# Kernel optimization log

Hardware: AMD Instinct MI355X
Metric: run time of the kernel (lower is better)

Reference implementation:

```python
import jax, jax.numpy as jnp
import numpy as np
import math

D_MODEL = 256
N_HEADS = 8
NUM_NODES = 20
KSIZE = 3
EPS = 1e-5


def _ln(x, g, b):
    m = jnp.mean(x, axis=-1, keepdims=True)
    v = jnp.mean(jnp.square(x - m), axis=-1, keepdims=True)
    return (x - m) * jax.lax.rsqrt(v + EPS) * g + b


def _conv1d(x_bdn, w_oik):
    # x: [B, D, N], w: [O, I, K], SAME padding, no bias
    return jax.lax.conv_general_dilated(
        x_bdn, w_oik, window_strides=(1,), padding='SAME',
        dimension_numbers=('NCH', 'OIH', 'NCH'))


def setup_inputs() -> dict:
    key = jax.random.key(0)
    ks = jax.random.split(key, 12)
    B, N, D, H, K = 8192, NUM_NODES, D_MODEL, N_HEADS, KSIZE
    s = 1.0 / math.sqrt(D * K)
    inp = {
        'x': jax.random.normal(ks[0], (B, N, D), jnp.float32),
        'wq': jax.random.normal(ks[1], (D, D, K), jnp.float32) * s,
        'wk': jax.random.normal(ks[2], (D, D, K), jnp.float32) * s,
        'wv': jax.random.normal(ks[3], (D, D, K), jnp.float32) * s,
        'gq': jnp.ones((D,), jnp.float32), 'bq': jnp.zeros((D,), jnp.float32),
        'gk': jnp.ones((D,), jnp.float32), 'bk': jnp.zeros((D,), jnp.float32),
        'gv': jnp.ones((D,), jnp.float32), 'bv': jnp.zeros((D,), jnp.float32),
        'rel_table': jax.random.normal(ks[4], (2 * N - 1, H), jnp.float32) * 0.02,
        'gbias': jax.random.normal(ks[5], (H, N, N), jnp.float32) * 0.02,
        'alpha': jnp.float32(1.0),
        'wo': jax.random.normal(ks[6], (D, D), jnp.float32) * (1.0 / math.sqrt(D)),
        'bo': jnp.zeros((D,), jnp.float32),
    }
    return inp


def reference(x, wq, wk, wv, gq, bq, gk, bk, gv, bv, rel_table, gbias, alpha, wo, bo):
    B, N, D = x.shape
    H = N_HEADS
    dk = D // H
    xp = jnp.transpose(x, (0, 2, 1))  # [B, D, N]
    q = x + _ln(jnp.transpose(_conv1d(xp, wq), (0, 2, 1)), gq, bq)
    k = x + _ln(jnp.transpose(_conv1d(xp, wk), (0, 2, 1)), gk, bk)
    v = x + _ln(jnp.transpose(_conv1d(xp, wv), (0, 2, 1)), gv, bv)
    q = q.reshape(B, N, H, dk).transpose(0, 2, 1, 3)  # [B, H, N, dk]
    k = k.reshape(B, N, H, dk).transpose(0, 2, 1, 3)
    v = v.reshape(B, N, H, dk).transpose(0, 2, 1, 3)
    scores = jnp.einsum('bhnd,bhmd->bhnm', q, k) / math.sqrt(dk)
    # relative position bias: index table [2N-1, H] -> [1, H, N, N]
    coords = jnp.arange(N)
    rel_idx = coords[:, None] - coords[None, :] + N - 1  # [N, N]
    rel_bias = rel_table[rel_idx]  # [N, N, H]
    scores = scores + jnp.transpose(rel_bias, (2, 0, 1))[None]
    scores = scores + gbias[None] * alpha
    attn = jax.nn.softmax(scores, axis=-1)
    out = jnp.einsum('bhnm,bhmd->bhnd', attn, v)  # dropout p=0
    out = out.transpose(0, 2, 1, 3).reshape(B, N, D)
    return out @ wo.T + bo
```

## Files before the change

kernel.cpp:

```cpp
#include <hip/hip_runtime.h>
#include <hip/hip_bf16.h>
#include <stdint.h>

#define BATCH 8192
#define NNODE 20
#define MROWS 163840
#define KCONV 768
#define NCONV 768
#define QSCALE 0.17677669529663687f

typedef __bf16 bf16x8 __attribute__((ext_vector_type(8)));
typedef float f32x4 __attribute__((ext_vector_type(4)));
typedef unsigned short u16x8 __attribute__((ext_vector_type(8)));

#define GLOBAL_AS __attribute__((address_space(1)))
#define LDS_AS __attribute__((address_space(3)))

__device__ __forceinline__ void load_lds16(const void* g, void* l) {
  __builtin_amdgcn_global_load_lds((const GLOBAL_AS uint32_t*)g,
                                   (LDS_AS uint32_t*)l, 16, 0, 0);
}

__device__ __forceinline__ float bf2f(unsigned short u) {
  union { unsigned int i; float f; } x;
  x.i = ((unsigned int)u) << 16;
  return x.f;
}

__global__ void prep_kernel(const float* __restrict__ x,
                            const float* __restrict__ wq,
                            const float* __restrict__ wk,
                            const float* __restrict__ wv,
                            const float* __restrict__ wo,
                            __hip_bfloat16* __restrict__ xb,
                            __hip_bfloat16* __restrict__ WcT,
                            __hip_bfloat16* __restrict__ wob,
                            int* __restrict__ zrow) {
  const int stride = gridDim.x * blockDim.x;
  const int gid = blockIdx.x * blockDim.x + threadIdx.x;

  if (gid < 128) zrow[gid] = 0;

  const int n8 = (MROWS * 256) / 8;
  for (int i8 = gid; i8 < n8; i8 += stride) {
    const float4* xp = ((const float4*)x) + (size_t)i8 * 2;
    float4 a = xp[0];
    float4 b = xp[1];
    __align__(16) __hip_bfloat16 h[8];
    h[0] = __float2bfloat16(a.x); h[1] = __float2bfloat16(a.y);
    h[2] = __float2bfloat16(a.z); h[3] = __float2bfloat16(a.w);
    h[4] = __float2bfloat16(b.x); h[5] = __float2bfloat16(b.y);
    h[6] = __float2bfloat16(b.z); h[7] = __float2bfloat16(b.w);
    ((int4*)xb)[i8] = *(const int4*)h;
  }

  for (int idx = gid; idx < NCONV * KCONV; idx += stride) {
    int n = idx / KCONV;
    int j = idx - n * KCONV;
    int c = n >> 8, o = n & 255;
    int t = j >> 8, i = j & 255;
    const float* w = (c == 0) ? wq : (c == 1) ? wk : wv;
    WcT[idx] = __float2bfloat16(w[(o * 256 + i) * 3 + t]);
  }

  for (int idx = gid; idx < 256 * 256; idx += stride) {
    wob[idx] = __float2bfloat16(wo[idx]);
  }
}

__global__ __launch_bounds__(512, 2) void conv_gemm_kernel(
    const __hip_bfloat16* __restrict__ xb,
    const __hip_bfloat16* __restrict__ WcT,
    __hip_bfloat16* __restrict__ y,
    const __hip_bfloat16* __restrict__ zrow) {
  __shared__ __align__(16) __hip_bfloat16 As[3][256 * 64];
  __shared__ __align__(16) __hip_bfloat16 Bs[3][128 * 64];

  const int tid = threadIdx.x;
  const int lane = tid & 63;
  const int wave = tid >> 6;
  const int wr = (wave >> 1) << 6;
  const int wc = (wave & 1) << 6;
  const int l16 = lane & 15;
  const int quad = lane >> 4;

  const int bid = blockIdx.x;
  const int xcd = bid & 7;
  const int g = xcd * 480 + (bid >> 3);
  const int mt = g / 6;
  const int nt = g - mt * 6;
  const int m0 = mt * 256;
  const int n0 = nt * 128;

  const __hip_bfloat16* a_base[4];
  const __hip_bfloat16* z_base[4];
  int a_node[4];
  int a_lds[4];
#pragma unroll
  for (int it = 0; it < 4; ++it) {
    int flat = tid + it * 512;
    int row = flat >> 3;
    int seg = flat & 7;
    int seg_g = seg ^ (row & 7);
    int gr = m0 + row;
    int b = gr / 20;
    a_node[it] = gr - b * 20;
    a_base[it] = xb + (long)(gr - 1) * 256 + seg_g * 8;
    z_base[it] = zrow + seg_g * 8;
    a_lds[it] = flat * 8;
  }
  const __hip_bfloat16* b_base[2];
  int b_lds[2];
#pragma unroll
  for (int it = 0; it < 2; ++it) {
    int flat = tid + it * 512;
    int row = flat >> 3;
    int seg = flat & 7;
    int seg_g = seg ^ (row & 7);
    b_base[it] = WcT + (size_t)(n0 + row) * KCONV + seg_g * 8;
    b_lds[it] = flat * 8;
  }

#define STAGE(KT, BUF)                                                        \
  {                                                                           \
    const int t_ = (KT) >> 2;                                                 \
    const int i0_ = ((KT) & 3) << 6;                                          \
    _Pragma("unroll") for (int it = 0; it < 4; ++it) {                        \
      bool ok = (unsigned)(a_node[it] + t_ - 1) < 20u;                        \
      const __hip_bfloat16* ga =                                              \
          ok ? (a_base[it] + t_ * 256 + i0_) : z_base[it];                    \
      load_lds16(ga, &As[BUF][a_lds[it]]);                                    \
    }                                                                         \
    _Pragma("unroll") for (int it = 0; it < 2; ++it) {                        \
      load_lds16(b_base[it] + (KT) * 64, &Bs[BUF][b_lds[it]]);                \
    }                                                                         \
  }

  f32x4 acc[4][4];
  const f32x4 zero = {0.f, 0.f, 0.f, 0.f};
#pragma unroll
  for (int i = 0; i < 4; ++i)
#pragma unroll
    for (int j = 0; j < 4; ++j) acc[i][j] = zero;

  STAGE(0, 0);
  STAGE(1, 1);
  asm volatile("s_waitcnt vmcnt(6)" ::: "memory");
  __builtin_amdgcn_s_barrier();
  __builtin_amdgcn_sched_barrier(0);

#pragma unroll
  for (int kt = 0; kt < 12; ++kt) {
    const int bc = kt % 3;
    if (kt < 10) {
      const int bs = (kt + 2) % 3;
      STAGE(kt + 2, bs);
    }
#pragma unroll
    for (int kk = 0; kk < 64; kk += 32) {
      const int sx = (((kk >> 3) + quad) ^ (l16 & 7)) << 3;
      bf16x8 af[4], bfr[4];
#pragma unroll
      for (int i = 0; i < 4; ++i)
        af[i] = *(const bf16x8*)&As[bc][((wr + i * 16 + l16) << 6) + sx];
#pragma unroll
      for (int j = 0; j < 4; ++j)
        bfr[j] = *(const bf16x8*)&Bs[bc][((wc + j * 16 + l16) << 6) + sx];
      __builtin_amdgcn_s_setprio(1);
#pragma unroll
      for (int i = 0; i < 4; ++i)
#pragma unroll
        for (int j = 0; j < 4; ++j)
          acc[i][j] = __builtin_amdgcn_mfma_f32_16x16x32_bf16(af[i], bfr[j],
                                                              acc[i][j], 0, 0, 0);
      __builtin_amdgcn_s_setprio(0);
    }
    if (kt < 10) {
      asm volatile("s_waitcnt vmcnt(6)" ::: "memory");
    } else if (kt == 10) {
      asm volatile("s_waitcnt vmcnt(0)" ::: "memory");
    }
    if (kt < 11) {
      __builtin_amdgcn_s_barrier();
      __builtin_amdgcn_sched_barrier(0);
    }
  }
#undef STAGE

#pragma unroll
  for (int i = 0; i < 4; ++i)
#pragma unroll
    for (int j = 0; j < 4; ++j)
#pragma unroll
      for (int r = 0; r < 4; ++r) {
        int row = m0 + wr + i * 16 + quad * 4 + r;
        int col = n0 + wc + j * 16 + l16;
        y[(size_t)row * NCONV + col] = __float2bfloat16(acc[i][j][r]);
      }
}

#define YST 776
__global__ __launch_bounds__(256) void attn5_kernel(
    const __hip_bfloat16* __restrict__ y,
    const __hip_bfloat16* __restrict__ xb,
    const float* __restrict__ rel,
    const float* __restrict__ gbias,
    const float* __restrict__ alpha_p,
    const float* __restrict__ gq, const float* __restrict__ bq,
    const float* __restrict__ gk, const float* __restrict__ bk,
    const float* __restrict__ gv, const float* __restrict__ bv,
    __hip_bfloat16* __restrict__ ao) {
  __shared__ __align__(16) __hip_bfloat16 yS[20 * YST];

  const int b = blockIdx.x;
  const int tid = threadIdx.x;
  const float alpha = alpha_p[0];
  const int lane = tid & 63;
  const int wave = tid >> 6;
  const int l16 = lane & 15;
  const int quad = lane >> 4;
  const f32x4 zero = {0.f, 0.f, 0.f, 0.f};

  const int4* src4 = (const int4*)(y + (size_t)b * NNODE * 768);
#pragma unroll
  for (int p = 0; p < 8; ++p) {
    int idx = tid + p * 256;
    if (idx < 1920) {
      int r = idx / 96;
      int c = idx - r * 96;
      *(int4*)&yS[r * YST + c * 8] = src4[idx];
    }
  }
  u16x8 xr[8];
  if (tid < 240) {
    const int rc = tid >> 2;
    const int p = tid & 3;
    const int r = rc / 3;
    const unsigned short* xp =
        (const unsigned short*)&xb[(((size_t)b * NNODE + r)) << 8];
#pragma unroll
    for (int s = 0; s < 8; ++s) xr[s] = *(const u16x8*)&xp[(s * 4 + p) * 8];
  }
  __syncthreads();

  if (tid < 240) {
    const int rc = tid >> 2;
    const int p = tid & 3;
    const int r = rc / 3;
    const int c = rc - r * 3;
    unsigned short* lp = (unsigned short*)&yS[r * YST + c * 256];

    float sum = 0.f, sq = 0.f;
#pragma unroll
    for (int s = 0; s < 8; ++s) {
      u16x8 v = *(const u16x8*)&lp[(s * 4 + p) * 8];
#pragma unroll
      for (int e = 0; e < 8; ++e) {
        float t = bf2f(v[e]);
        sum += t;
        sq += t * t;
      }
    }
    sum += __shfl_xor(sum, 1, 64); sq += __shfl_xor(sq, 1, 64);
    sum += __shfl_xor(sum, 2, 64); sq += __shfl_xor(sq, 2, 64);

    const float mean = sum * (1.0f / 256.0f);
    const float var = sq * (1.0f / 256.0f) - mean * mean;
    const float rstd = rsqrtf(var + 1e-5f);
    const float osc = (c == 0) ? QSCALE : 1.0f;

    const float* g = (c == 0) ? gq : (c == 1) ? gk : gv;
    const float* bb = (c == 0) ? bq : (c == 1) ? bk : bv;

#pragma unroll
    for (int s = 0; s < 8; ++s) {
      const int c0 = (s * 4 + p) * 8;
      u16x8 v = *(const u16x8*)&lp[c0];
      u16x8 xv = xr[s];
      float4 g0 = *(const float4*)&g[c0];
      float4 g1 = *(const float4*)&g[c0 + 4];
      float4 b0 = *(const float4*)&bb[c0];
      float4 b1 = *(const float4*)&bb[c0 + 4];
      const float* gf0 = (const float*)&g0;
      const float* gf1 = (const float*)&g1;
      const float* bf0 = (const float*)&b0;
      const float* bf1 = (const float*)&b1;
      __align__(16) __hip_bfloat16 h[8];
#pragma unroll
      for (int e = 0; e < 4; ++e)
        h[e] = __float2bfloat16(
            (bf2f(xv[e]) + (bf2f(v[e]) - mean) * rstd * gf0[e] + bf0[e]) * osc);
#pragma unroll
      for (int e = 0; e < 4; ++e)
        h[4 + e] = __float2bfloat16(
            (bf2f(xv[4 + e]) + (bf2f(v[4 + e]) - mean) * rstd * gf1[e] + bf1[e]) * osc);
      *(int4*)&lp[c0] = *(const int4*)h;
    }
  }
  __syncthreads();

  const unsigned short* ySu = (const unsigned short*)yS;
#pragma unroll
  for (int hh = 0; hh < 2; ++hh) {
    const int h = wave * 2 + hh;
    const int rlo = l16;
    const int rhi = (l16 + 16 < 20) ? (l16 + 16) : 19;

    bf16x8 kf0 = *(const bf16x8*)&yS[rlo * YST + 256 + h * 32 + quad * 8];
    bf16x8 kf1 = *(const bf16x8*)&yS[rhi * YST + 256 + h * 32 + quad * 8];
    bf16x8 qf0 = *(const bf16x8*)&yS[rlo * YST + h * 32 + quad * 8];
    bf16x8 qf1 = *(const bf16x8*)&yS[rhi * YST + h * 32 + quad * 8];

    f32x4 c00, c01, c10, c11;
    {
      const float4 g00 = *(const float4*)&gbias[h * 400 + rlo * 20 + quad * 4];
      const float4 g01 = *(const float4*)&gbias[h * 400 + rhi * 20 + quad * 4];
#pragma unroll
      for (int r = 0; r < 4; ++r) {
        const int j0 = quad * 4 + r;
        const int j1 = (16 + j0 < 20) ? (16 + j0) : 19;
        c00[r] = alpha * ((const float*)&g00)[r] + rel[(rlo - j0 + 19) * 8 + h];
        c01[r] = alpha * ((const float*)&g01)[r] + rel[(rhi - j0 + 19) * 8 + h];
        c10[r] = alpha * gbias[h * 400 + rlo * 20 + j1] + rel[(rlo - j1 + 19) * 8 + h];
        c11[r] = alpha * gbias[h * 400 + rhi * 20 + j1] + rel[(rhi - j1 + 19) * 8 + h];
      }
    }
    c00 = __builtin_amdgcn_mfma_f32_16x16x32_bf16(kf0, qf0, c00, 0, 0, 0);
    c01 = __builtin_amdgcn_mfma_f32_16x16x32_bf16(kf0, qf1, c01, 0, 0, 0);
    c10 = __builtin_amdgcn_mfma_f32_16x16x32_bf16(kf1, qf0, c10, 0, 0, 0);
    c11 = __builtin_amdgcn_mfma_f32_16x16x32_bf16(kf1, qf1, c11, 0, 0, 0);

    float p00[4], p10[4], p01[4], p11[4];
    {
      float m = fmaxf(fmaxf(c00[0], c00[1]), fmaxf(c00[2], c00[3]));
      if (quad == 0)
        m = fmaxf(m, fmaxf(fmaxf(c10[0], c10[1]), fmaxf(c10[2], c10[3])));
      m = fmaxf(m, __shfl_xor(m, 16, 64));
      m = fmaxf(m, __shfl_xor(m, 32, 64));
      float s = 0.f;
#pragma unroll
      for (int r = 0; r < 4; ++r) { p00[r] = __expf(c00[r] - m); s += p00[r]; }
#pragma unroll
      for (int r = 0; r < 4; ++r) {
        p10[r] = (quad == 0) ? __expf(c10[r] - m) : 0.f;
        s += p10[r];
      }
      s += __shfl_xor(s, 16, 64);
      s += __shfl_xor(s, 32, 64);
      const float inv = 1.0f / s;
#pragma unroll
      for (int r = 0; r < 4; ++r) { p00[r] *= inv; p10[r] *= inv; }
    }
    {
      float m = fmaxf(fmaxf(c01[0], c01[1]), fmaxf(c01[2], c01[3]));
      if (quad == 0)
        m = fmaxf(m, fmaxf(fmaxf(c11[0], c11[1]), fmaxf(c11[2], c11[3])));
      m = fmaxf(m, __shfl_xor(m, 16, 64));
      m = fmaxf(m, __shfl_xor(m, 32, 64));
      float s = 0.f;
#pragma unroll
      for (int r = 0; r < 4; ++r) { p01[r] = __expf(c01[r] - m); s += p01[r]; }
#pragma unroll
      for (int r = 0; r < 4; ++r) {
        p11[r] = (quad == 0) ? __expf(c11[r] - m) : 0.f;
        s += p11[r];
      }
      s += __shfl_xor(s, 16, 64);
      s += __shfl_xor(s, 32, 64);
      const float inv = 1.0f / s;
#pragma unroll
      for (int r = 0; r < 4; ++r) { p01[r] *= inv; p11[r] *= inv; }
    }

    const int srcA = ((quad * 2) & 3) * 16 + l16;
    const int srcB = ((quad * 2 + 1) & 3) * 16 + l16;
    __align__(16) __hip_bfloat16 aLo[8], aHi[8];
#pragma unroll
    for (int r = 0; r < 4; ++r) {
      float xa = __shfl(p00[r], srcA, 64);
      float xc = __shfl(p00[r], srcB, 64);
      float xt = __shfl(p10[r], l16, 64);
      float lo = (quad < 2) ? xa : ((quad == 2) ? xt : 0.f);
      float hi = (quad < 2) ? xc : 0.f;
      aLo[r] = __float2bfloat16(lo);
      aLo[4 + r] = __float2bfloat16(hi);
      float ya = __shfl(p01[r], srcA, 64);
      float yc = __shfl(p01[r], srcB, 64);
      float yt = __shfl(p11[r], l16, 64);
      lo = (quad < 2) ? ya : ((quad == 2) ? yt : 0.f);
      hi = (quad < 2) ? yc : 0.f;
      aHi[r] = __float2bfloat16(lo);
      aHi[4 + r] = __float2bfloat16(hi);
    }

    __align__(16) __hip_bfloat16 bv0[8], bv1[8];
#pragma unroll
    for (int e = 0; e < 8; ++e) {
      int jj = quad * 8 + e;
      int jc = (jj < 20) ? jj : 19;
      const __hip_bfloat16* vp =
          (const __hip_bfloat16*)&ySu[jc * YST + 512 + h * 32];
      bv0[e] = vp[l16];
      bv1[e] = vp[16 + l16];
    }

    f32x4 d00 = __builtin_amdgcn_mfma_f32_16x16x32_bf16(
        *(const bf16x8*)aLo, *(const bf16x8*)bv0, zero, 0, 0, 0);
    f32x4 d01 = __builtin_amdgcn_mfma_f32_16x16x32_bf16(
        *(const bf16x8*)aLo, *(const bf16x8*)bv1, zero, 0, 0, 0);
    f32x4 d10 = __builtin_amdgcn_mfma_f32_16x16x32_bf16(
        *(const bf16x8*)aHi, *(const bf16x8*)bv0, zero, 0, 0, 0);
    f32x4 d11 = __builtin_amdgcn_mfma_f32_16x16x32_bf16(
        *(const bf16x8*)aHi, *(const bf16x8*)bv1, zero, 0, 0, 0);

    __hip_bfloat16* aob = ao + (((size_t)(b * 20)) << 8) + h * 32;
#pragma unroll
    for (int r = 0; r < 4; ++r) {
      const int i0 = quad * 4 + r;
      aob[i0 * 256 + l16] = __float2bfloat16(d00[r]);
      aob[i0 * 256 + 16 + l16] = __float2bfloat16(d01[r]);
      const int i1 = 16 + i0;
      if (i1 < 20) {
        aob[i1 * 256 + l16] = __float2bfloat16(d10[r]);
        aob[i1 * 256 + 16 + l16] = __float2bfloat16(d11[r]);
      }
    }
  }
}

__global__ __launch_bounds__(256) void proj_gemm_kernel(
    const __hip_bfloat16* __restrict__ ao,
    const __hip_bfloat16* __restrict__ wob,
    const float* __restrict__ bo,
    float* __restrict__ out) {
  __shared__ __align__(16) __hip_bfloat16 As[128 * 64];
  __shared__ __align__(16) __hip_bfloat16 Bs[128 * 64];

  const int tid = threadIdx.x;
  const int lane = tid & 63;
  const int wave = tid >> 6;
  const int wm = (wave >> 1) << 6;
  const int wn = (wave & 1) << 6;
  const int l16 = lane & 15;
  const int quad = lane >> 4;

  const int bid = blockIdx.x;
  const int xcd = bid & 7;
  const int q = bid >> 3;
  const int m0 = (xcd * 160 + (q >> 1)) * 128;
  const int n0 = (q & 1) * 128;

  const __hip_bfloat16* a_base[4];
  const __hip_bfloat16* b_base[4];
  int lds_off[4];
#pragma unroll
  for (int it = 0; it < 4; ++it) {
    int flat = ((it * 4 + wave) << 6) + lane;
    int row = flat >> 3;
    int seg = flat & 7;
    int seg_g = seg ^ (row & 7);
    a_base[it] = ao + (((size_t)(m0 + row)) << 8) + seg_g * 8;
    b_base[it] = wob + (((size_t)(n0 + row)) << 8) + seg_g * 8;
    lds_off[it] = (it * 4 + wave) << 9;
  }

  f32x4 acc[4][4];
  const f32x4 zero = {0.f, 0.f, 0.f, 0.f};
#pragma unroll
  for (int i = 0; i < 4; ++i)
#pragma unroll
    for (int j = 0; j < 4; ++j) acc[i][j] = zero;

  for (int kt = 0; kt < 4; ++kt) {
    const int k0 = kt << 6;
#pragma unroll
    for (int it = 0; it < 4; ++it) {
      load_lds16(a_base[it] + k0, &As[lds_off[it]]);
      load_lds16(b_base[it] + k0, &Bs[lds_off[it]]);
    }
    __syncthreads();

#pragma unroll
    for (int kk = 0; kk < 64; kk += 32) {
      const int sx = (((kk >> 3) + quad) ^ (l16 & 7)) << 3;
      bf16x8 af[4], bfr[4];
#pragma unroll
      for (int i = 0; i < 4; ++i)
        af[i] = *(const bf16x8*)&As[((wm + i * 16 + l16) << 6) + sx];
#pragma unroll
      for (int j = 0; j < 4; ++j)
        bfr[j] = *(const bf16x8*)&Bs[((wn + j * 16 + l16) << 6) + sx];
#pragma unroll
      for (int i = 0; i < 4; ++i)
#pragma unroll
        for (int j = 0; j < 4; ++j)
          acc[i][j] = __builtin_amdgcn_mfma_f32_16x16x32_bf16(af[i], bfr[j],
                                                              acc[i][j], 0, 0, 0);
    }
    __syncthreads();
  }

#pragma unroll
  for (int i = 0; i < 4; ++i)
#pragma unroll
    for (int j = 0; j < 4; ++j) {
      int col = n0 + wn + j * 16 + l16;
      float bias = bo[col];
#pragma unroll
      for (int r = 0; r < 4; ++r) {
        int row = m0 + wm + i * 16 + quad * 4 + r;
        out[(size_t)row * 256 + col] = acc[i][j][r] + bias;
      }
    }
}

extern "C" void kernel_launch(void* const* d_in, const int* in_sizes, int n_in,
                              void* d_out, int out_size, void* d_ws, size_t ws_size,
                              hipStream_t stream) {
  const float* x     = (const float*)d_in[0];
  const float* wq    = (const float*)d_in[1];
  const float* wk    = (const float*)d_in[2];
  const float* wv    = (const float*)d_in[3];
  const float* gq    = (const float*)d_in[4];
  const float* bq    = (const float*)d_in[5];
  const float* gk    = (const float*)d_in[6];
  const float* bk    = (const float*)d_in[7];
  const float* gv    = (const float*)d_in[8];
  const float* bv    = (const float*)d_in[9];
  const float* rel   = (const float*)d_in[10];
  const float* gbias = (const float*)d_in[11];
  const float* alpha = (const float*)d_in[12];
  const float* wo    = (const float*)d_in[13];
  const float* bo    = (const float*)d_in[14];
  float* out = (float*)d_out;

  char* ws = (char*)d_ws;
  __hip_bfloat16* xb  = (__hip_bfloat16*)(ws);
  __hip_bfloat16* y   = (__hip_bfloat16*)(ws + 83886080);
  __hip_bfloat16* ao  = (__hip_bfloat16*)(ws + 335544320);
  __hip_bfloat16* WcT = (__hip_bfloat16*)(ws + 419430400);
  __hip_bfloat16* wob = (__hip_bfloat16*)(ws + 420610048);
  int*            zr  = (int*)(ws + 420741120);

  prep_kernel<<<8192, 256, 0, stream>>>(x, wq, wk, wv, wo, xb, WcT, wob, zr);
  conv_gemm_kernel<<<3840, 512, 0, stream>>>(xb, WcT, y,
                                             (const __hip_bfloat16*)zr);
  attn5_kernel<<<8192, 256, 0, stream>>>(y, xb, rel, gbias, alpha,
                                         gq, bq, gk, bk, gv, bv, ao);
  proj_gemm_kernel<<<2560, 256, 0, stream>>>(ao, wob, bo, out);
}
```

Baseline: 773.6 us.

## Load conv GEMM weight fragments directly to registers instead of LDS staging

The B operand (conv weights) is no longer staged through LDS. Each lane now loads its MFMA B fragments directly from global memory into registers, double-buffered across k-steps, while the A tile keeps its triple-buffered LDS pipeline. This frees 48KB of LDS and removes the LDS reads for B, which could raise occupancy and cut LDS traffic. In exchange it adds VGPR pressure and uncoalesced 16-byte global loads, which should mostly hit cache because the weights are small. The vmcnt accounting is retuned to match, which is delicate now that B loads and LDS-direct A loads share the same counter.

```diff
diff --git a/kernel.cpp b/kernel.cpp
--- a/kernel.cpp
+++ b/kernel.cpp
@@ -74,7 +74,6 @@
     __hip_bfloat16* __restrict__ y,
     const __hip_bfloat16* __restrict__ zrow) {
   __shared__ __align__(16) __hip_bfloat16 As[3][256 * 64];
-  __shared__ __align__(16) __hip_bfloat16 Bs[3][128 * 64];
 
   const int tid = threadIdx.x;
   const int lane = tid & 63;
@@ -109,19 +108,13 @@
     z_base[it] = zrow + seg_g * 8;
     a_lds[it] = flat * 8;
   }
-  const __hip_bfloat16* b_base[2];
-  int b_lds[2];
-#pragma unroll
-  for (int it = 0; it < 2; ++it) {
-    int flat = tid + it * 512;
-    int row = flat >> 3;
-    int seg = flat & 7;
-    int seg_g = seg ^ (row & 7);
-    b_base[it] = WcT + (size_t)(n0 + row) * KCONV + seg_g * 8;
-    b_lds[it] = flat * 8;
-  }
-
-#define STAGE(KT, BUF)                                                        \
+
+  const __hip_bfloat16* wrow[4];
+#pragma unroll
+  for (int j = 0; j < 4; ++j)
+    wrow[j] = WcT + (size_t)(n0 + wc + j * 16 + l16) * KCONV + quad * 8;
+
+#define STAGE_A(KT, BUF)                                                      \
   {                                                                           \
     const int t_ = (KT) >> 2;                                                 \
     const int i0_ = ((KT) & 3) << 6;                                          \
@@ -131,9 +124,36 @@
           ok ? (a_base[it] + t_ * 256 + i0_) : z_base[it];                    \
       load_lds16(ga, &As[BUF][a_lds[it]]);                                    \
     }                                                                         \
-    _Pragma("unroll") for (int it = 0; it < 2; ++it) {                        \
-      load_lds16(b_base[it] + (KT) * 64, &Bs[BUF][b_lds[it]]);                \
+  }
+
+#define LOADB(KT, B0, B1)                                                     \
+  {                                                                           \
+    _Pragma("unroll") for (int j = 0; j < 4; ++j) {                           \
+      B0[j] = *(const bf16x8*)(wrow[j] + (KT) * 64);                          \
+      B1[j] = *(const bf16x8*)(wrow[j] + (KT) * 64 + 32);                     \
     }                                                                         \
+  }
+
+#define COMPUTE(KT, B0, B1)                                                   \
+  {                                                                           \
+    const int bc_ = (KT) % 3;                                                 \
+    const int sx0_ = (quad ^ (l16 & 7)) << 3;                                 \
+    const int sx1_ = ((4 + quad) ^ (l16 & 7)) << 3;                           \
+    bf16x8 af0[4], af1[4];                                                    \
+    _Pragma("unroll") for (int i = 0; i < 4; ++i) {                           \
+      af0[i] = *(const bf16x8*)&As[bc_][((wr + i * 16 + l16) << 6) + sx0_];   \
+      af1[i] = *(const bf16x8*)&As[bc_][((wr + i * 16 + l16) << 6) + sx1_];   \
+    }                                                                         \
+    __builtin_amdgcn_s_setprio(1);                                            \
+    _Pragma("unroll") for (int i = 0; i < 4; ++i)                             \
+        _Pragma("unroll") for (int j = 0; j < 4; ++j)                         \
+            acc[i][j] = __builtin_amdgcn_mfma_f32_16x16x32_bf16(              \
+                af0[i], B0[j], acc[i][j], 0, 0, 0);                           \
+    _Pragma("unroll") for (int i = 0; i < 4; ++i)                             \
+        _Pragma("unroll") for (int j = 0; j < 4; ++j)                         \
+            acc[i][j] = __builtin_amdgcn_mfma_f32_16x16x32_bf16(              \
+                af1[i], B1[j], acc[i][j], 0, 0, 0);                           \
+    __builtin_amdgcn_s_setprio(0);                                            \
   }
 
   f32x4 acc[4][4];
@@ -143,40 +163,34 @@
 #pragma unroll
     for (int j = 0; j < 4; ++j) acc[i][j] = zero;
 
-  STAGE(0, 0);
-  STAGE(1, 1);
-  asm volatile("s_waitcnt vmcnt(6)" ::: "memory");
+  bf16x8 bEv0[4], bEv1[4], bOd0[4], bOd1[4];
+
+  STAGE_A(0, 0);
+  LOADB(0, bEv0, bEv1);
+  STAGE_A(1, 1);
+  asm volatile("s_waitcnt vmcnt(4)" ::: "memory");
   __builtin_amdgcn_s_barrier();
   __builtin_amdgcn_sched_barrier(0);
 
 #pragma unroll
   for (int kt = 0; kt < 12; ++kt) {
-    const int bc = kt % 3;
+    if (kt + 1 < 12) {
+      if ((kt + 1) & 1) {
+        LOADB(kt + 1, bOd0, bOd1);
+      } else {
+        LOADB(kt + 1, bEv0, bEv1);
+      }
+    }
+    if (kt + 2 < 12) {
+      STAGE_A(kt + 2, (kt + 2) % 3);
+    }
+    if (kt & 1) {
+      COMPUTE(kt, bOd0, bOd1);
+    } else {
+      COMPUTE(kt, bEv0, bEv1);
+    }
     if (kt < 10) {
-      const int bs = (kt + 2) % 3;
-      STAGE(kt + 2, bs);
-    }
-#pragma unroll
-    for (int kk = 0; kk < 64; kk += 32) {
-      const int sx = (((kk >> 3) + quad) ^ (l16 & 7)) << 3;
-      bf16x8 af[4], bfr[4];
-#pragma unroll
-      for (int i = 0; i < 4; ++i)
-        af[i] = *(const bf16x8*)&As[bc][((wr + i * 16 + l16) << 6) + sx];
-#pragma unroll
-      for (int j = 0; j < 4; ++j)
-        bfr[j] = *(const bf16x8*)&Bs[bc][((wc + j * 16 + l16) << 6) + sx];
-      __builtin_amdgcn_s_setprio(1);
-#pragma unroll
-      for (int i = 0; i < 4; ++i)
-#pragma unroll
-        for (int j = 0; j < 4; ++j)
-          acc[i][j] = __builtin_amdgcn_mfma_f32_16x16x32_bf16(af[i], bfr[j],
-                                                              acc[i][j], 0, 0, 0);
-      __builtin_amdgcn_s_setprio(0);
-    }
-    if (kt < 10) {
-      asm volatile("s_waitcnt vmcnt(6)" ::: "memory");
+      asm volatile("s_waitcnt vmcnt(4)" ::: "memory");
     } else if (kt == 10) {
       asm volatile("s_waitcnt vmcnt(0)" ::: "memory");
     }
@@ -185,7 +199,9 @@
       __builtin_amdgcn_sched_barrier(0);
     }
   }
-#undef STAGE
+#undef STAGE_A
+#undef LOADB
+#undef COMPUTE
 
 #pragma unroll
   for (int i = 0; i < 4; ++i)
```

After: 1.002 ms. 29.5% more time.
